# Performance work log

Measured on AMD Instinct MI355X. Metric: run time of the kernel, lower is better.

The kernel has to match this reference:

```python
import jax, jax.numpy as jnp
import numpy as np


def setup_inputs() -> dict:
    key = jax.random.key(0)
    ks = jax.random.split(key, 6)
    B, S, D, F, E = 4, 2048, 512, 2048, 8
    scale = 0.02
    return {
        "x": jax.random.normal(ks[0], (B, S, D), dtype=jnp.float32),
        "gate_w": jax.random.normal(ks[1], (D, E), dtype=jnp.float32) * scale,
        "w1": jax.random.normal(ks[2], (E, D, F), dtype=jnp.float32) * scale,
        "b1": jax.random.normal(ks[3], (E, F), dtype=jnp.float32) * scale,
        "w2": jax.random.normal(ks[4], (E, F, D), dtype=jnp.float32) * scale,
        "b2": jax.random.normal(ks[5], (E, D), dtype=jnp.float32) * scale,
    }


TOP_K = 2


def reference(x, gate_w, w1, b1, w2, b2):
    E = w1.shape[0]
    orig_shape = x.shape
    xr = x.reshape(-1, x.shape[-1])              # [T, D]

    # Router
    logits = xr @ gate_w                          # [T, E]
    probs = jax.nn.softmax(logits, axis=-1)
    mean_probs = probs.mean(axis=0)               # [E]
    load_balance_loss = E * jnp.sum(mean_probs * mean_probs)

    topw, topi = jax.lax.top_k(probs, TOP_K)      # [T, K]
    topw = topw / jnp.sum(topw, axis=-1, keepdims=True)

    # Per-token combine weight per expert: sum over top-k slots of weight * one-hot
    combine = jnp.sum(jax.nn.one_hot(topi, E, dtype=xr.dtype) * topw[..., None], axis=1)  # [T, E]

    # Dense per-expert FFN (equivalent math to the permute/slice dispatch:
    # each selected token gets expert_e(x) scaled by its normalized router weight).
    hidden = jax.nn.gelu(jnp.einsum("td,edf->etf", xr, w1) + b1[:, None, :], approximate=False)  # [E, T, F]
    outs = jnp.einsum("etf,efd->etd", hidden, w2) + b2[:, None, :]                               # [E, T, D]

    y = jnp.einsum("etd,te->td", outs, combine)   # [T, D]
    return y.reshape(orig_shape), load_balance_loss
```

## Files before the change

kernel.cpp:

```cpp
#include <hip/hip_runtime.h>
#include <stdint.h>

#define T_TOKENS 8192
#define D_DIM 512
#define F_DIM 2048
#define E_NUM 8

typedef short short8 __attribute__((ext_vector_type(8)));
typedef float f32x4 __attribute__((ext_vector_type(4)));

__device__ __forceinline__ unsigned short f2bf(float f) {
    union { float f; unsigned int u; } c; c.f = f;
    unsigned int u = c.u;
    unsigned int r = (u + 0x7fffu + ((u >> 16) & 1u)) >> 16;
    return (unsigned short)r;
}
__device__ __forceinline__ unsigned int pack2(float a, float b) {
    return (unsigned int)f2bf(a) | ((unsigned int)f2bf(b) << 16);
}
__device__ __forceinline__ float gelu_fast(float h) {
    float a = h * fmaf(h * h, -0.0713548162f, -1.5957691216f);
    return h / (1.f + __expf(a));
}

#define SLOT_CAP 17408
#define WS_COUNT 0
#define WS_PROBS 512
#define WS_TOK   16384
#define WS_WGT   (WS_TOK + E_NUM * T_TOKENS * 4)
#define WS_INV   (WS_WGT + E_NUM * T_TOKENS * 4)
#define WS_W1B   (1ull << 20)
#define WS_W2B   (WS_W1B + 16777216ull)
#define WS_XG    (WS_W2B + 16777216ull)
#define WS_HG    (WS_XG + (unsigned long long)SLOT_CAP * D_DIM * 2)
#define WS_OG    (WS_HG + (unsigned long long)SLOT_CAP * F_DIM * 2)

__device__ __forceinline__ void expert_off(const int* __restrict__ count, int e,
                                           int& off_e, int& cnt_e) {
    int off = 0, ce = 0;
#pragma unroll
    for (int i = 0; i < E_NUM; ++i) {
        int c = count[i];
        if (i == e) ce = c;
        if (i < e) off += (c + 127) & ~127;
    }
    off_e = off; cnt_e = ce;
}

__global__ __launch_bounds__(256) void moe_convert(
    const float* __restrict__ w1, const float* __restrict__ w2,
    unsigned short* __restrict__ w1b, unsigned short* __restrict__ w2b,
    int* __restrict__ count, float* __restrict__ probs_g)
{
    __shared__ float ts[32][65];
    int tid = threadIdx.x;
    if (blockIdx.x == 0 && tid < E_NUM) { count[tid] = 0; probs_g[tid] = 0.f; }

    int b = blockIdx.x;
    bool is2 = b >= 4096;
    int o = is2 ? b - 4096 : b;
    int e = o >> 9, r = o & 511;
    int N  = is2 ? 512 : 2048;
    int Ks = is2 ? 64 : 16;
    int ng, ks;
    if (!is2) { ng = r & 31; ks = r >> 5; }
    else      { ng = r & 7;  ks = r >> 3; }

    const float* src = (is2 ? w2 : w1) + ((size_t)e << 20) + (size_t)(ks * 32) * N + ng * 64;
    int row = tid >> 3, c4 = (tid & 7) * 4;
    f32x4 v0 = *(const f32x4*)(src + (size_t)row * N + c4);
    f32x4 v1 = *(const f32x4*)(src + (size_t)row * N + c4 + 32);
    *(f32x4*)&ts[row][c4] = v0;
    *(f32x4*)&ts[row][c4 + 32] = v1;
    __syncthreads();

    int f = tid >> 6, L = tid & 63, q = L >> 4, n = L & 15;
    float v[8];
#pragma unroll
    for (int j = 0; j < 8; ++j) v[j] = ts[q * 8 + j][f * 16 + n];
    uint4 pk;
    pk.x = pack2(v[0], v[1]); pk.y = pack2(v[2], v[3]);
    pk.z = pack2(v[4], v[5]); pk.w = pack2(v[6], v[7]);
    size_t fraglane = ((size_t)((e * (N / 16) + ng * 4 + f) * Ks + ks)) * 64 + L;
    unsigned short* dst = (is2 ? w2b : w1b) + fraglane * 8;
    *(uint4*)dst = pk;
}

__global__ __launch_bounds__(256) void moe_router(
    const float* __restrict__ x, const float* __restrict__ gw,
    int* __restrict__ count, int* __restrict__ tok_list,
    float* __restrict__ wgt_list, float* __restrict__ probs_g,
    int* __restrict__ inv)
{
    __shared__ float pprob[E_NUM];
    __shared__ int   lcnt[E_NUM];
    __shared__ int   gbase[E_NUM];
    __shared__ int   ltok[E_NUM][64];
    __shared__ float lwgt[E_NUM][64];
    __shared__ unsigned char re1[32], re2[32];
    __shared__ short rs1[32], rs2[32];

    int tid = threadIdx.x;
    if (tid < E_NUM) { pprob[tid] = 0.f; lcnt[tid] = 0; }
    __syncthreads();

    int wv = tid >> 6, lane = tid & 63;

    float gr[64];
    {
        const f32x4* gp = (const f32x4*)(gw + lane * 64);
#pragma unroll
        for (int i = 0; i < 16; ++i) *(f32x4*)&gr[i * 4] = gp[i];
    }

    float wps[E_NUM];
#pragma unroll
    for (int e = 0; e < E_NUM; ++e) wps[e] = 0.f;

#pragma unroll 1
    for (int i = 0; i < 8; ++i) {
        int t = blockIdx.x * 32 + wv * 8 + i;
        const float* xp = x + (size_t)t * D_DIM + lane * 8;
        f32x4 x0 = *(const f32x4*)xp;
        f32x4 x1 = *(const f32x4*)(xp + 4);
        float xv[8] = { x0.x, x0.y, x0.z, x0.w, x1.x, x1.y, x1.z, x1.w };
        float acc[E_NUM];
#pragma unroll
        for (int e = 0; e < E_NUM; ++e) acc[e] = 0.f;
#pragma unroll
        for (int j = 0; j < 8; ++j)
#pragma unroll
            for (int e = 0; e < E_NUM; ++e) acc[e] += xv[j] * gr[j * 8 + e];
#pragma unroll
        for (int off = 1; off < 64; off <<= 1)
#pragma unroll
            for (int e = 0; e < E_NUM; ++e) acc[e] += __shfl_xor(acc[e], off);

        float m = acc[0];
#pragma unroll
        for (int e = 1; e < E_NUM; ++e) m = fmaxf(m, acc[e]);
        float p[E_NUM], s = 0.f;
#pragma unroll
        for (int e = 0; e < E_NUM; ++e) { p[e] = __expf(acc[e] - m); s += p[e]; }
        float invs = 1.f / s;
#pragma unroll
        for (int e = 0; e < E_NUM; ++e) { p[e] *= invs; wps[e] += p[e]; }

        int e1 = 0;
#pragma unroll
        for (int e = 1; e < E_NUM; ++e) if (p[e] > p[e1]) e1 = e;
        int e2 = (e1 == 0) ? 1 : 0;
#pragma unroll
        for (int e = 0; e < E_NUM; ++e) if (e != e1 && p[e] > p[e2]) e2 = e;

        if (lane == 0) {
            float invw = 1.f / (p[e1] + p[e2]);
            int s1 = atomicAdd(&lcnt[e1], 1); ltok[e1][s1] = t; lwgt[e1][s1] = p[e1] * invw;
            int s2 = atomicAdd(&lcnt[e2], 1); ltok[e2][s2] = t; lwgt[e2][s2] = p[e2] * invw;
            int li = wv * 8 + i;
            re1[li] = (unsigned char)e1; rs1[li] = (short)s1;
            re2[li] = (unsigned char)e2; rs2[li] = (short)s2;
        }
    }
    if (lane == 0) {
#pragma unroll
        for (int e = 0; e < E_NUM; ++e) atomicAdd(&pprob[e], wps[e]);
    }
    __syncthreads();
    if (tid < E_NUM) {
        gbase[tid] = atomicAdd(&count[tid], lcnt[tid]);
        atomicAdd(&probs_g[tid], pprob[tid]);
    }
    __syncthreads();
    if (tid < 32) {
        int t = blockIdx.x * 32 + tid;
        inv[t * 2]     = ((int)re1[tid] << 16) | (gbase[re1[tid]] + rs1[tid]);
        inv[t * 2 + 1] = ((int)re2[tid] << 16) | (gbase[re2[tid]] + rs2[tid]);
    }
    int ee = tid >> 5;
    for (int ss = tid & 31; ss < lcnt[ee]; ss += 32) {
        int dst = ee * T_TOKENS + gbase[ee] + ss;
        tok_list[dst] = ltok[ee][ss];
        wgt_list[dst] = lwgt[ee][ss];
    }
}

__global__ __launch_bounds__(256) void moe_gather(
    const float* __restrict__ x, const int* __restrict__ count,
    const int* __restrict__ tok_list, unsigned short* __restrict__ Xg,
    const float* __restrict__ probs_g, float* __restrict__ y)
{
    if (blockIdx.x == 0 && threadIdx.x == 0) {
        float s = 0.f;
#pragma unroll
        for (int i = 0; i < E_NUM; ++i) {
            float m = probs_g[i] / (float)T_TOKENS;
            s += m * m;
        }
        y[(size_t)T_TOKENS * D_DIM] = (float)E_NUM * s;
    }

    int e = blockIdx.x & 7, tile = blockIdx.x >> 3;
    int off_e, cnt;
    expert_off(count, e, off_e, cnt);
    int padcnt = (cnt + 127) & ~127;
    if (tile * 64 >= padcnt) return;

    int tid = threadIdx.x;
    int tl = tid >> 2;
    int kq = tid & 3;
    int slot = tile * 64 + tl;
    bool valid = slot < cnt;
    int tok = valid ? tok_list[e * T_TOKENS + slot] : 0;
    const float* xr = x + (size_t)tok * D_DIM + kq * 128;
    int base16 = ((off_e + tile * 64) >> 4) + (tl >> 4);
    int mlane = tl & 15;

#pragma unroll 4
    for (int g = 0; g < 16; ++g) {
        uint4 pk;
        if (valid) {
            f32x4 v0 = *(const f32x4*)(xr + g * 8);
            f32x4 v1 = *(const f32x4*)(xr + g * 8 + 4);
            pk.x = pack2(v0.x, v0.y); pk.y = pack2(v0.z, v0.w);
            pk.z = pack2(v1.x, v1.y); pk.w = pack2(v1.z, v1.w);
        } else {
            pk.x = 0; pk.y = 0; pk.z = 0; pk.w = 0;
        }
        int kb = kq * 4 + (g >> 2);
        int lane = mlane + 16 * (g & 3);
        *(uint4*)(Xg + ((size_t)(base16 * 16 + kb) * 64 + lane) * 8) = pk;
    }
}

__global__ __launch_bounds__(256) void moe_gemm1(
    const unsigned short* __restrict__ Xg, const unsigned short* __restrict__ w1b,
    const float* __restrict__ b1, const int* __restrict__ count,
    unsigned short* __restrict__ Hg)
{
    int e = blockIdx.x & 7;
    int r = blockIdx.x >> 3;
    int mt = r >> 4, nt = r & 15;
    int off_e, cnt;
    expert_off(count, e, off_e, cnt);
    if (mt * 128 >= cnt) return;

    __shared__ unsigned short us[4][64][72];

    int tid = threadIdx.x;
    int wv = tid >> 6, lane = tid & 63;
    int wh = wv >> 1, nh = wv & 1;
    int q = lane >> 4, n = lane & 15;

    int slot16b = (off_e >> 4) + mt * 8 + wh * 4;
    const short8* Ap = (const short8*)Xg + (size_t)slot16b * 1024 + lane;
    const short8* Bp = (const short8*)w1b + (size_t)(e * 128 + nt * 8 + nh * 4) * 1024 + lane;

    f32x4 acc[4][4];
#pragma unroll
    for (int j = 0; j < 4; ++j)
#pragma unroll
        for (int i = 0; i < 4; ++i) acc[j][i] = (f32x4){0.f, 0.f, 0.f, 0.f};

#pragma unroll 2
    for (int ks = 0; ks < 16; ++ks) {
        short8 A[4], B[4];
#pragma unroll
        for (int i = 0; i < 4; ++i) A[i] = Ap[(size_t)i * 1024 + ks * 64];
#pragma unroll
        for (int j = 0; j < 4; ++j) B[j] = Bp[(size_t)j * 1024 + ks * 64];
#pragma unroll
        for (int j = 0; j < 4; ++j)
#pragma unroll
            for (int i = 0; i < 4; ++i)
                acc[j][i] = __builtin_amdgcn_mfma_f32_16x16x32_bf16(A[i], B[j], acc[j][i], 0, 0, 0);
    }

#pragma unroll
    for (int j = 0; j < 4; ++j) {
        float bb = b1[e * F_DIM + (nt * 8 + nh * 4 + j) * 16 + n];
#pragma unroll
        for (int i = 0; i < 4; ++i)
#pragma unroll
            for (int rr = 0; rr < 4; ++rr)
                us[wv][i * 16 + q * 4 + rr][j * 16 + n] = f2bf(gelu_fast(acc[j][i][rr] + bb));
    }
    __syncthreads();

#pragma unroll
    for (int i = 0; i < 4; ++i)
#pragma unroll
        for (int kb = 0; kb < 2; ++kb) {
            short8 v = *(const short8*)&us[wv][i * 16 + n][kb * 32 + q * 8];
            size_t idx = ((size_t)(slot16b + i) * 64 + (nt * 4 + nh * 2 + kb)) * 64 + lane;
            *(short8*)((unsigned short*)Hg + idx * 8) = v;
        }
}

__global__ __launch_bounds__(256) void moe_gemm2(
    const unsigned short* __restrict__ Hg, const unsigned short* __restrict__ w2b,
    const float* __restrict__ b2, const int* __restrict__ count,
    const float* __restrict__ wgt_list, float* __restrict__ Og)
{
    int e = blockIdx.x & 7;
    int r = blockIdx.x >> 3;
    int mt = r >> 2, nt = r & 3;
    int off_e, cnt;
    expert_off(count, e, off_e, cnt);
    if (mt * 128 >= cnt) return;

    __shared__ float swgt[128];

    int tid = threadIdx.x;
    if (tid < 128) {
        int s = mt * 128 + tid;
        swgt[tid] = (s < cnt) ? wgt_list[e * T_TOKENS + s] : 0.f;
    }
    __syncthreads();

    int wv = tid >> 6, lane = tid & 63;
    int wh = wv >> 1, nh = wv & 1;
    int q = lane >> 4, n = lane & 15;

    int slot16b = (off_e >> 4) + mt * 8 + wh * 4;
    const short8* Ap = (const short8*)Hg + (size_t)slot16b * 4096 + lane;
    const short8* Bp = (const short8*)w2b + (size_t)(e * 32 + nt * 8 + nh * 4) * 4096 + lane;

    f32x4 acc[4][4];
#pragma unroll
    for (int j = 0; j < 4; ++j)
#pragma unroll
        for (int i = 0; i < 4; ++i) acc[j][i] = (f32x4){0.f, 0.f, 0.f, 0.f};

#pragma unroll 2
    for (int kb = 0; kb < 64; ++kb) {
        short8 A[4], B[4];
#pragma unroll
        for (int i = 0; i < 4; ++i) A[i] = Ap[(size_t)i * 4096 + kb * 64];
#pragma unroll
        for (int j = 0; j < 4; ++j) B[j] = Bp[(size_t)j * 4096 + kb * 64];
#pragma unroll
        for (int j = 0; j < 4; ++j)
#pragma unroll
            for (int i = 0; i < 4; ++i)
                acc[j][i] = __builtin_amdgcn_mfma_f32_16x16x32_bf16(A[i], B[j], acc[j][i], 0, 0, 0);
    }

    float* orow = Og + (size_t)(off_e + mt * 128) * D_DIM;
#pragma unroll
    for (int j = 0; j < 4; ++j) {
        int d = (nt * 8 + nh * 4 + j) * 16 + n;
        float bb = b2[e * D_DIM + d];
#pragma unroll
        for (int i = 0; i < 4; ++i)
#pragma unroll
            for (int rr = 0; rr < 4; ++rr) {
                int m = wh * 64 + i * 16 + q * 4 + rr;
                orow[(size_t)m * D_DIM + d] = swgt[m] * (acc[j][i][rr] + bb);
            }
    }
}

__global__ __launch_bounds__(256) void moe_combine(
    const float* __restrict__ Og, const int* __restrict__ inv,
    const int* __restrict__ count, float* __restrict__ y)
{
    __shared__ int offs[E_NUM];
    int tid = threadIdx.x;
    if (tid < E_NUM) {
        int off = 0;
        for (int i = 0; i < tid; ++i) off += (count[i] + 127) & ~127;
        offs[tid] = off;
    }
    __syncthreads();

    int tk = blockIdx.x * 2 + (tid >> 7);
    int l = tid & 127;
    int i1 = inv[tk * 2], i2 = inv[tk * 2 + 1];
    int e1 = i1 >> 16, g1 = i1 & 0xffff;
    int e2 = i2 >> 16, g2 = i2 & 0xffff;
    f32x4 a = *((const f32x4*)(Og + (size_t)(offs[e1] + g1) * D_DIM) + l);
    f32x4 b = *((const f32x4*)(Og + (size_t)(offs[e2] + g2) * D_DIM) + l);
    f32x4 o = { a.x + b.x, a.y + b.y, a.z + b.z, a.w + b.w };
    *((f32x4*)(y + (size_t)tk * D_DIM) + l) = o;
}

extern "C" void kernel_launch(void* const* d_in, const int* in_sizes, int n_in,
                              void* d_out, int out_size, void* d_ws, size_t ws_size,
                              hipStream_t stream) {
    const float* x  = (const float*)d_in[0];
    const float* gw = (const float*)d_in[1];
    const float* w1 = (const float*)d_in[2];
    const float* b1 = (const float*)d_in[3];
    const float* w2 = (const float*)d_in[4];
    const float* b2 = (const float*)d_in[5];
    float* out = (float*)d_out;

    char* ws = (char*)d_ws;
    int*   count     = (int*)(ws + WS_COUNT);
    float* probs_g   = (float*)(ws + WS_PROBS);
    int*   tok_list  = (int*)(ws + WS_TOK);
    float* wgt_list  = (float*)(ws + WS_WGT);
    int*   inv       = (int*)(ws + WS_INV);
    unsigned short* w1b = (unsigned short*)(ws + WS_W1B);
    unsigned short* w2b = (unsigned short*)(ws + WS_W2B);
    unsigned short* Xg  = (unsigned short*)(ws + WS_XG);
    unsigned short* Hg  = (unsigned short*)(ws + WS_HG);
    float*          Og  = (float*)(ws + WS_OG);

    moe_convert<<<8192, 256, 0, stream>>>(w1, w2, w1b, w2b, count, probs_g);
    moe_router<<<T_TOKENS / 32, 256, 0, stream>>>(x, gw, count, tok_list, wgt_list, probs_g, inv);
    moe_gather<<<8 * 128, 256, 0, stream>>>(x, count, tok_list, Xg, probs_g, out);
    moe_gemm1<<<8 * 64 * 16, 256, 0, stream>>>(Xg, w1b, b1, count, Hg);
    moe_gemm2<<<8 * 64 * 4, 256, 0, stream>>>(Hg, w2b, b2, count, wgt_list, Og);
    moe_combine<<<T_TOKENS / 2, 256, 0, stream>>>(Og, inv, count, out);
}
```

Measured before the change: 299.9 us.

## Stage GEMM operand tiles through LDS with direct global-to-LDS loads

Both expert GEMM kernels now cooperatively load A and B tiles into shared memory using global_load_lds, so each wave reads operands from LDS instead of each wave fetching its own fragments straight from global memory. This removes the duplicate global loads where pairs of waves shared the same A or B rows. The cost is two barriers per K step with no double buffering, so load latency is no longer overlapped with MFMA work. The LDS buffer is also reused for the GELU epilogue in gemm1.

```diff
diff --git a/kernel.cpp b/kernel.cpp
--- a/kernel.cpp
+++ b/kernel.cpp
@@ -21,6 +21,12 @@
 __device__ __forceinline__ float gelu_fast(float h) {
     float a = h * fmaf(h * h, -0.0713548162f, -1.5957691216f);
     return h / (1.f + __expf(a));
+}
+
+__device__ __forceinline__ void gload_lds16(const void* g, void* l) {
+    __builtin_amdgcn_global_load_lds(
+        (const __attribute__((address_space(1))) void*)g,
+        (__attribute__((address_space(3))) void*)l, 16, 0, 0);
 }
 
 #define SLOT_CAP 17408
@@ -245,16 +251,18 @@
     expert_off(count, e, off_e, cnt);
     if (mt * 128 >= cnt) return;
 
-    __shared__ unsigned short us[4][64][72];
+    __shared__ __align__(16) unsigned short smem[4 * 64 * 72];
+    unsigned short* Alds = smem;
+    unsigned short* Blds = smem + 8192;
 
     int tid = threadIdx.x;
     int wv = tid >> 6, lane = tid & 63;
     int wh = wv >> 1, nh = wv & 1;
     int q = lane >> 4, n = lane & 15;
 
-    int slot16b = (off_e >> 4) + mt * 8 + wh * 4;
-    const short8* Ap = (const short8*)Xg + (size_t)slot16b * 1024 + lane;
-    const short8* Bp = (const short8*)w1b + (size_t)(e * 128 + nt * 8 + nh * 4) * 1024 + lane;
+    int slot16b = (off_e >> 4) + mt * 8;
+    const short8* Ag8 = (const short8*)Xg + (size_t)slot16b * 1024;
+    const short8* Bg8 = (const short8*)w1b + (size_t)(e * 128 + nt * 8) * 1024;
 
     f32x4 acc[4][4];
 #pragma unroll
@@ -262,20 +270,42 @@
 #pragma unroll
         for (int i = 0; i < 4; ++i) acc[j][i] = (f32x4){0.f, 0.f, 0.f, 0.f};
 
-#pragma unroll 2
-    for (int ks = 0; ks < 16; ++ks) {
-        short8 A[4], B[4];
-#pragma unroll
-        for (int i = 0; i < 4; ++i) A[i] = Ap[(size_t)i * 1024 + ks * 64];
-#pragma unroll
-        for (int j = 0; j < 4; ++j) B[j] = Bp[(size_t)j * 1024 + ks * 64];
-#pragma unroll
-        for (int j = 0; j < 4; ++j)
+    int isB = wv >> 1;
+    const short8* Sg = isB ? Bg8 : Ag8;
+    unsigned short* Sl = isB ? Blds : Alds;
+    int half = wv & 1;
+
+#pragma unroll 1
+    for (int kt = 0; kt < 8; ++kt) {
+#pragma unroll
+        for (int rr = 0; rr < 8; ++rr) {
+            int idx = half * 8 + rr;
+            int s = idx >> 1, kbi = idx & 1;
+            const short8* g = Sg + (size_t)s * 1024 + (kt * 2 + kbi) * 64 + lane;
+            unsigned short* l = Sl + (size_t)((s * 2 + kbi) * 64) * 8;
+            gload_lds16((const void*)g, (void*)l);
+        }
+        __syncthreads();
+
+#pragma unroll
+        for (int kbi = 0; kbi < 2; ++kbi) {
+            short8 A[4], B[4];
 #pragma unroll
             for (int i = 0; i < 4; ++i)
-                acc[j][i] = __builtin_amdgcn_mfma_f32_16x16x32_bf16(A[i], B[j], acc[j][i], 0, 0, 0);
-    }
-
+                A[i] = *(const short8*)(Alds + (size_t)((((wh * 4 + i) * 2 + kbi) * 64 + lane)) * 8);
+#pragma unroll
+            for (int j = 0; j < 4; ++j)
+                B[j] = *(const short8*)(Blds + (size_t)((((nh * 4 + j) * 2 + kbi) * 64 + lane)) * 8);
+#pragma unroll
+            for (int j = 0; j < 4; ++j)
+#pragma unroll
+                for (int i = 0; i < 4; ++i)
+                    acc[j][i] = __builtin_amdgcn_mfma_f32_16x16x32_bf16(A[i], B[j], acc[j][i], 0, 0, 0);
+        }
+        __syncthreads();
+    }
+
+    unsigned short* us = smem + wv * 4608;
 #pragma unroll
     for (int j = 0; j < 4; ++j) {
         float bb = b1[e * F_DIM + (nt * 8 + nh * 4 + j) * 16 + n];
@@ -283,16 +313,15 @@
         for (int i = 0; i < 4; ++i)
 #pragma unroll
             for (int rr = 0; rr < 4; ++rr)
-                us[wv][i * 16 + q * 4 + rr][j * 16 + n] = f2bf(gelu_fast(acc[j][i][rr] + bb));
-    }
-    __syncthreads();
+                us[(i * 16 + q * 4 + rr) * 72 + j * 16 + n] = f2bf(gelu_fast(acc[j][i][rr] + bb));
+    }
 
 #pragma unroll
     for (int i = 0; i < 4; ++i)
 #pragma unroll
         for (int kb = 0; kb < 2; ++kb) {
-            short8 v = *(const short8*)&us[wv][i * 16 + n][kb * 32 + q * 8];
-            size_t idx = ((size_t)(slot16b + i) * 64 + (nt * 4 + nh * 2 + kb)) * 64 + lane;
+            short8 v = *(const short8*)(us + (size_t)(i * 16 + n) * 72 + kb * 32 + q * 8);
+            size_t idx = ((size_t)(slot16b + wh * 4 + i) * 64 + (nt * 4 + nh * 2 + kb)) * 64 + lane;
             *(short8*)((unsigned short*)Hg + idx * 8) = v;
         }
 }
@@ -309,6 +338,9 @@
     expert_off(count, e, off_e, cnt);
     if (mt * 128 >= cnt) return;
 
+    __shared__ __align__(16) unsigned short smem[16384];
+    unsigned short* Alds = smem;
+    unsigned short* Blds = smem + 8192;
     __shared__ float swgt[128];
 
     int tid = threadIdx.x;
@@ -316,15 +348,14 @@
         int s = mt * 128 + tid;
         swgt[tid] = (s < cnt) ? wgt_list[e * T_TOKENS + s] : 0.f;
     }
-    __syncthreads();
 
     int wv = tid >> 6, lane = tid & 63;
     int wh = wv >> 1, nh = wv & 1;
     int q = lane >> 4, n = lane & 15;
 
-    int slot16b = (off_e >> 4) + mt * 8 + wh * 4;
-    const short8* Ap = (const short8*)Hg + (size_t)slot16b * 4096 + lane;
-    const short8* Bp = (const short8*)w2b + (size_t)(e * 32 + nt * 8 + nh * 4) * 4096 + lane;
+    int slot16b = (off_e >> 4) + mt * 8;
+    const short8* Ag8 = (const short8*)Hg + (size_t)slot16b * 4096;
+    const short8* Bg8 = (const short8*)w2b + (size_t)(e * 32 + nt * 8) * 4096;
 
     f32x4 acc[4][4];
 #pragma unroll
@@ -332,18 +363,39 @@
 #pragma unroll
         for (int i = 0; i < 4; ++i) acc[j][i] = (f32x4){0.f, 0.f, 0.f, 0.f};
 
-#pragma unroll 2
-    for (int kb = 0; kb < 64; ++kb) {
-        short8 A[4], B[4];
-#pragma unroll
-        for (int i = 0; i < 4; ++i) A[i] = Ap[(size_t)i * 4096 + kb * 64];
-#pragma unroll
-        for (int j = 0; j < 4; ++j) B[j] = Bp[(size_t)j * 4096 + kb * 64];
-#pragma unroll
-        for (int j = 0; j < 4; ++j)
+    int isB = wv >> 1;
+    const short8* Sg = isB ? Bg8 : Ag8;
+    unsigned short* Sl = isB ? Blds : Alds;
+    int half = wv & 1;
+
+#pragma unroll 1
+    for (int kt = 0; kt < 32; ++kt) {
+#pragma unroll
+        for (int rr = 0; rr < 8; ++rr) {
+            int idx = half * 8 + rr;
+            int s = idx >> 1, kbi = idx & 1;
+            const short8* g = Sg + (size_t)s * 4096 + (kt * 2 + kbi) * 64 + lane;
+            unsigned short* l = Sl + (size_t)((s * 2 + kbi) * 64) * 8;
+            gload_lds16((const void*)g, (void*)l);
+        }
+        __syncthreads();
+
+#pragma unroll
+        for (int kbi = 0; kbi < 2; ++kbi) {
+            short8 A[4], B[4];
 #pragma unroll
             for (int i = 0; i < 4; ++i)
-                acc[j][i] = __builtin_amdgcn_mfma_f32_16x16x32_bf16(A[i], B[j], acc[j][i], 0, 0, 0);
+                A[i] = *(const short8*)(Alds + (size_t)((((wh * 4 + i) * 2 + kbi) * 64 + lane)) * 8);
+#pragma unroll
+            for (int j = 0; j < 4; ++j)
+                B[j] = *(const short8*)(Blds + (size_t)((((nh * 4 + j) * 2 + kbi) * 64 + lane)) * 8);
+#pragma unroll
+            for (int j = 0; j < 4; ++j)
+#pragma unroll
+                for (int i = 0; i < 4; ++i)
+                    acc[j][i] = __builtin_amdgcn_mfma_f32_16x16x32_bf16(A[i], B[j], acc[j][i], 0, 0, 0);
+        }
+        __syncthreads();
     }
 
     float* orow = Og + (size_t)(off_e + mt * 128) * D_DIM;
```

Result: no change. 301.1 us (+0.4%).

## Write GEMM1 hidden output directly via transposed MFMA, drop LDS staging

Applied to the files above, without the earlier changes.

GEMM1 swaps the MFMA operands so each lane holds four consecutive F values for one token. It then writes 8-byte chunks of the hidden activations straight to global memory in a new interleaved layout, removing the shared-memory transpose and its barrier. GEMM2 is adapted to read this layout as two 8-byte loads per A fragment, which costs more, narrower loads in the hot loop. The GELU divide is also replaced by a hardware reciprocal.

```diff
diff --git a/kernel.cpp b/kernel.cpp
--- a/kernel.cpp
+++ b/kernel.cpp
@@ -7,6 +7,7 @@
 #define E_NUM 8
 
 typedef short short8 __attribute__((ext_vector_type(8)));
+typedef short s16x4 __attribute__((ext_vector_type(4)));
 typedef float f32x4 __attribute__((ext_vector_type(4)));
 
 __device__ __forceinline__ unsigned short f2bf(float f) {
@@ -20,7 +21,7 @@
 }
 __device__ __forceinline__ float gelu_fast(float h) {
     float a = h * fmaf(h * h, -0.0713548162f, -1.5957691216f);
-    return h / (1.f + __expf(a));
+    return h * __builtin_amdgcn_rcpf(1.f + __expf(a));
 }
 
 #define SLOT_CAP 17408
@@ -245,8 +246,6 @@
     expert_off(count, e, off_e, cnt);
     if (mt * 128 >= cnt) return;
 
-    __shared__ unsigned short us[4][64][72];
-
     int tid = threadIdx.x;
     int wv = tid >> 6, lane = tid & 63;
     int wh = wv >> 1, nh = wv & 1;
@@ -273,28 +272,23 @@
         for (int j = 0; j < 4; ++j)
 #pragma unroll
             for (int i = 0; i < 4; ++i)
-                acc[j][i] = __builtin_amdgcn_mfma_f32_16x16x32_bf16(A[i], B[j], acc[j][i], 0, 0, 0);
-    }
-
+                acc[j][i] = __builtin_amdgcn_mfma_f32_16x16x32_bf16(B[j], A[i], acc[j][i], 0, 0, 0);
+    }
+
+    s16x4* Hg8 = (s16x4*)Hg;
 #pragma unroll
     for (int j = 0; j < 4; ++j) {
-        float bb = b1[e * F_DIM + (nt * 8 + nh * 4 + j) * 16 + n];
-#pragma unroll
-        for (int i = 0; i < 4; ++i)
+        f32x4 bb = *(const f32x4*)(b1 + e * F_DIM + nt * 128 + nh * 64 + j * 16 + q * 4);
+        int cfb = nt * 32 + nh * 16 + j * 4;
+#pragma unroll
+        for (int i = 0; i < 4; ++i) {
+            s16x4 sv;
 #pragma unroll
             for (int rr = 0; rr < 4; ++rr)
-                us[wv][i * 16 + q * 4 + rr][j * 16 + n] = f2bf(gelu_fast(acc[j][i][rr] + bb));
-    }
-    __syncthreads();
-
-#pragma unroll
-    for (int i = 0; i < 4; ++i)
-#pragma unroll
-        for (int kb = 0; kb < 2; ++kb) {
-            short8 v = *(const short8*)&us[wv][i * 16 + n][kb * 32 + q * 8];
-            size_t idx = ((size_t)(slot16b + i) * 64 + (nt * 4 + nh * 2 + kb)) * 64 + lane;
-            *(short8*)((unsigned short*)Hg + idx * 8) = v;
+                sv[rr] = (short)f2bf(gelu_fast(acc[j][i][rr] + bb[rr]));
+            Hg8[(size_t)(slot16b + i) * 8192 + cfb * 16 + lane] = sv;
         }
+    }
 }
 
 __global__ __launch_bounds__(256) void moe_gemm2(
@@ -323,7 +317,7 @@
     int q = lane >> 4, n = lane & 15;
 
     int slot16b = (off_e >> 4) + mt * 8 + wh * 4;
-    const short8* Ap = (const short8*)Hg + (size_t)slot16b * 4096 + lane;
+    const s16x4* Ah = (const s16x4*)Hg + (size_t)slot16b * 8192 + q * 32 + n;
     const short8* Bp = (const short8*)w2b + (size_t)(e * 32 + nt * 8 + nh * 4) * 4096 + lane;
 
     f32x4 acc[4][4];
@@ -336,7 +330,11 @@
     for (int kb = 0; kb < 64; ++kb) {
         short8 A[4], B[4];
 #pragma unroll
-        for (int i = 0; i < 4; ++i) A[i] = Ap[(size_t)i * 4096 + kb * 64];
+        for (int i = 0; i < 4; ++i) {
+            s16x4 lo = Ah[(size_t)i * 8192 + kb * 128];
+            s16x4 hi = Ah[(size_t)i * 8192 + kb * 128 + 16];
+            A[i] = __builtin_shufflevector(lo, hi, 0, 1, 2, 3, 4, 5, 6, 7);
+        }
 #pragma unroll
         for (int j = 0; j < 4; ++j) B[j] = Bp[(size_t)j * 4096 + kb * 64];
 #pragma unroll
```

After: 311.9 us. 4.0% more time.
